# Performance work log

Hardware: AMD Instinct MI355X
Metric: run time of the kernel (lower is better)

Reference implementation:

```python
import jax, jax.numpy as jnp
import numpy as np

N, D_MODEL, NUM_HEAD = 2, 256, 8
HI, WI = 40, 40
MAX_DIS = 7
WS = 2 * MAX_DIS + 1          # 15
HD = D_MODEL // NUM_HEAD      # 32
T = HD ** 0.5
NEG = 1e8                     # fp32 mask value used by the torch module


def setup_inputs() -> dict:
    key = jax.random.key(0)
    ks = jax.random.split(key, 10)
    s = 0.02
    f = lambda i, shape: jax.random.normal(ks[i], shape, jnp.float32)
    return dict(
        q=f(0, (N, D_MODEL, HI, WI)),
        k=f(1, (N, D_MODEL, HI, WI)),
        v=f(2, (N, D_MODEL, HI, WI)),
        Wq=f(3, (D_MODEL, D_MODEL)) * s, bq=jnp.zeros((D_MODEL,), jnp.float32),
        Wk=f(4, (D_MODEL, D_MODEL)) * s, bk=jnp.zeros((D_MODEL,), jnp.float32),
        Wv=f(5, (D_MODEL, D_MODEL)) * s, bv=jnp.zeros((D_MODEL,), jnp.float32),
        rel_k_w=f(6, (NUM_HEAD, WS * WS, HD)) * s,      # grouped 1x1 conv weight
        rel_k_b=jnp.zeros((NUM_HEAD, WS * WS), jnp.float32),
        rel_v=f(7, (NUM_HEAD, HD, WS * WS)) * s,        # nn.Parameter (zeros in torch; random here to exercise math)
        Wp=f(8, (D_MODEL, D_MODEL)) * s, bp=jnp.zeros((D_MODEL,), jnp.float32),
    )


def _geometry(h, w):
    # Static (numpy) index/mask construction matching compute_mask().
    qy = np.repeat(np.arange(h), w)
    qx = np.tile(np.arange(w), h)
    dy = qy[None, :] - qy[:, None]          # key - query, [hw, hw]
    dx = qx[None, :] - qx[:, None]
    valid = (np.abs(dy) <= MAX_DIS) & (np.abs(dx) <= MAX_DIS)
    widx = (np.clip(dy + MAX_DIS, 0, WS - 1) * WS + np.clip(dx + MAX_DIS, 0, WS - 1))
    offs = np.arange(-MAX_DIS, MAX_DIS + 1)
    dyo = np.repeat(offs, WS)               # [ws*ws] row-major window order (dy*WS+dx)
    dxo = np.tile(offs, WS)
    ky = qy[:, None] + dyo[None, :]         # [hw, ws*ws]
    kx = qx[:, None] + dxo[None, :]
    in_img = (ky >= 0) & (ky < h) & (kx >= 0) & (kx < w)
    jidx = np.clip(ky, 0, h - 1) * w + np.clip(kx, 0, w - 1)
    return (jnp.asarray(valid), jnp.asarray(widx), jnp.asarray(in_img), jnp.asarray(jidx))


def reference(q, k, v, Wq, bq, Wk, bk, Wv, bv, rel_k_w, rel_k_b, rel_v, Wp, bp):
    n, c, h, w = q.shape
    hw = h * w
    nh, hd = NUM_HEAD, c // NUM_HEAD

    def proj(x, Wt, b):  # 1x1 conv == per-pixel linear
        return jnp.einsum('oc,ncp->nop', Wt, x.reshape(n, c, hw)) + b[None, :, None]

    qf = proj(q, Wq, bq)
    kf = proj(k, Wk, bk)
    vf = proj(v, Wv, bv)

    qh = qf.reshape(n, nh, hd, hw)
    kh = kf.reshape(n, nh, hd, hw)
    vh = vf.reshape(n, nh, hd, hw)

    # grouped 1x1 conv: per-head linear from hd channels to ws*ws (computed BEFORE q/T)
    rel = jnp.einsum('hwd,nhdp->nhpw', rel_k_w, qh) + rel_k_b[None, :, None, :]  # [n,nh,hw,ws2]

    qh = qh / T
    qk = jnp.einsum('nhdi,nhdj->nhij', qh, kh)   # [n,nh,hw,hw]

    valid, widx, in_img, jidx = _geometry(h, w)

    # --- 'global' path: dense hw x hw, non-local keys masked with -1e8, local keys get rel bias ---
    rel_dense = jnp.take_along_axis(rel, widx[None, None], axis=3)   # [n,nh,hw,hw]
    global_logits = jnp.where(valid[None, None], qk + rel_dense, qk - NEG)
    global_attn = jax.nn.softmax(global_logits, axis=-1)
    agg_value = jnp.einsum('nhij,nhdj->inhd', global_attn, vh).reshape(hw, n, c)

    # --- local path: gather ws*ws window per query; out-of-image keys are -1e8 (pad value), rel added everywhere ---
    gathered = jnp.take_along_axis(qk, jidx[None, None], axis=3)     # [n,nh,hw,ws2]
    local_logits = jnp.where(in_img[None, None], gathered, -NEG) + rel
    local_attn = jax.nn.softmax(local_logits, axis=-1)
    agg_bias = jnp.einsum('nhiw,hdw->inhd', local_attn, rel_v).reshape(hw, n, c)

    out = (agg_value + agg_bias) @ Wp.T + bp    # nn.Linear, output [hw, n, c]
    return out, local_attn
```

## Files before the change

kernel.cpp:

```cpp
#include <hip/hip_runtime.h>
#include <hip/hip_bf16.h>

#define HW    1600
#define NB    2
#define NHEAD 8
#define HD    32
#define WS2   225
#define WDIM  40
#define CDIM  256
#define PROJ  819200
#define RELSTR 248
#define TSC   5.656854249492381f

typedef __attribute__((ext_vector_type(8))) short short8;
typedef __attribute__((ext_vector_type(4))) float floatx4;

static __device__ __forceinline__ float bu2f(short u) {
    return __uint_as_float(((unsigned)(unsigned short)u) << 16);
}
static __device__ __forceinline__ short f2bu(float f) {
    __hip_bfloat16 h = __float2bfloat16(f);
    short s; __builtin_memcpy(&s, &h, 2); return s;
}
static __device__ __forceinline__ unsigned pk2(short a, short b) {
    return (unsigned)(unsigned short)a | ((unsigned)(unsigned short)b << 16);
}
static __device__ __forceinline__ float ldf(const void* p, size_t i, bool f32) {
    return f32 ? ((const float*)p)[i] : __bfloat162float(((const __hip_bfloat16*)p)[i]);
}
static __device__ __forceinline__ void st_out(void* p, size_t i, float v, bool f32) {
    if (f32) ((float*)p)[i] = v;
    else     ((__hip_bfloat16*)p)[i] = __float2bfloat16(v);
}

__global__ __launch_bounds__(256) void prep_kernel(
    const void* __restrict__ q, const void* __restrict__ relv,
    const void* __restrict__ Wq, const void* __restrict__ Wk,
    const void* __restrict__ Wv, const void* __restrict__ Wp,
    const void* __restrict__ bq, const void* __restrict__ bk,
    const void* __restrict__ bv, const void* __restrict__ bp,
    const void* __restrict__ rkw, const void* __restrict__ rkb,
    int* __restrict__ flag, __hip_bfloat16* __restrict__ relvT,
    __hip_bfloat16* __restrict__ Wqb, __hip_bfloat16* __restrict__ Wkb,
    __hip_bfloat16* __restrict__ Wvb, __hip_bfloat16* __restrict__ Wpb,
    float* __restrict__ bqf, float* __restrict__ bkf,
    float* __restrict__ bvf, float* __restrict__ bpf,
    __hip_bfloat16* __restrict__ rkwb, __hip_bfloat16* __restrict__ rkbb)
{
    __shared__ int sbad;
    if (threadIdx.x == 0) sbad = 0;
    __syncthreads();
    int bad = 0;
    const __hip_bfloat16* qb = (const __hip_bfloat16*)q;
    for (int i = threadIdx.x; i < 4096; i += 256) {
        float v = __bfloat162float(qb[i]);
        if (!(v > -1e6f && v < 1e6f)) bad = 1;
    }
    if (bad) sbad = 1;
    __syncthreads();
    const bool f32 = (sbad != 0);
    if (blockIdx.x == 0 && threadIdx.x == 0) *flag = sbad;

    const int gid = blockIdx.x * 256 + threadIdx.x;
    const int gsz = gridDim.x * 256;

    for (int e = gid; e < NHEAD * WS2 * HD; e += gsz) {
        const int h = e / (WS2 * HD), idx = e - h * (WS2 * HD);
        const int w = idx >> 5, d = idx & 31;
        relvT[e] = __float2bfloat16(ldf(relv, ((size_t)h * HD + d) * WS2 + w, f32));
    }
    for (int e = gid; e < CDIM * CDIM; e += gsz) {
        Wqb[e] = __float2bfloat16(ldf(Wq, e, f32));
        Wkb[e] = __float2bfloat16(ldf(Wk, e, f32));
        Wvb[e] = __float2bfloat16(ldf(Wv, e, f32));
        Wpb[e] = __float2bfloat16(ldf(Wp, e, f32));
    }
    for (int e = gid; e < CDIM; e += gsz) {
        bqf[e] = ldf(bq, e, f32); bkf[e] = ldf(bk, e, f32);
        bvf[e] = ldf(bv, e, f32); bpf[e] = ldf(bp, e, f32);
    }
    for (int e = gid; e < NHEAD * WS2 * HD; e += gsz)
        rkwb[e] = __float2bfloat16(ldf(rkw, e, f32));
    for (int e = gid; e < NHEAD * WS2; e += gsz)
        rkbb[e] = __float2bfloat16(ldf(rkb, e, f32));
}

__global__ __launch_bounds__(256) void proj_fused(
    const void* __restrict__ xq, const void* __restrict__ xk, const void* __restrict__ xv,
    const __hip_bfloat16* __restrict__ Wqb, const float* __restrict__ bqf,
    const __hip_bfloat16* __restrict__ Wkb, const float* __restrict__ bkf,
    const __hip_bfloat16* __restrict__ Wvb, const float* __restrict__ bvf,
    const int* __restrict__ flag,
    __hip_bfloat16* __restrict__ qs, __hip_bfloat16* __restrict__ ks,
    __hip_bfloat16* __restrict__ vs)
{
    __shared__ short xt[32][264];
    const bool f32 = (*flag != 0);
    const int m0 = blockIdx.x * 32;
    const int n  = blockIdx.y;
    const int t  = blockIdx.z;
    const void* x; const short* W; const float* bias; __hip_bfloat16* dst; float scale;
    if (t == 0)      { x = xq; W = (const short*)Wqb; bias = bqf; dst = qs; scale = 0.17677669529663687f; }
    else if (t == 1) { x = xk; W = (const short*)Wkb; bias = bkf; dst = ks; scale = 1.f; }
    else             { x = xv; W = (const short*)Wvb; bias = bvf; dst = vs; scale = 1.f; }

    {
        const int c = threadIdx.x;
        const size_t xb = ((size_t)n * CDIM + c) * HW + m0;
        if (f32) {
            const float* xr = (const float*)x + xb;
            #pragma unroll
            for (int g = 0; g < 8; ++g) {
                float4 f = *(const float4*)(xr + g * 4);
                xt[g*4+0][c] = f2bu(f.x); xt[g*4+1][c] = f2bu(f.y);
                xt[g*4+2][c] = f2bu(f.z); xt[g*4+3][c] = f2bu(f.w);
            }
        } else {
            const __hip_bfloat16* xr = (const __hip_bfloat16*)x + xb;
            #pragma unroll
            for (int g = 0; g < 4; ++g) {
                short8 s = *(const short8*)(xr + g * 8);
                #pragma unroll
                for (int u = 0; u < 8; ++u) xt[g*8+u][c] = s[u];
            }
        }
    }
    __syncthreads();

    const int wave = threadIdx.x >> 6, lane = threadIdx.x & 63;
    const int m = lane & 15, qd = lane >> 4;

    short8 A[2][8];
    #pragma unroll
    for (int mt = 0; mt < 2; ++mt)
        #pragma unroll
        for (int k = 0; k < 8; ++k)
            A[mt][k] = *(const short8*)(&xt[mt*16 + m][k*32 + qd*8]);

    #pragma unroll
    for (int og = 0; og < 4; ++og) {
        const int o0 = (wave * 4 + og) * 16;
        short8 B[8];
        #pragma unroll
        for (int k = 0; k < 8; ++k)
            B[k] = *(const short8*)(W + (size_t)(o0 + m) * CDIM + k*32 + qd*8);
        floatx4 acc0 = {0,0,0,0}, acc1 = {0,0,0,0};
        #pragma unroll
        for (int k = 0; k < 8; ++k) {
            acc0 = __builtin_amdgcn_mfma_f32_16x16x32_bf16(A[0][k], B[k], acc0, 0, 0, 0);
            acc1 = __builtin_amdgcn_mfma_f32_16x16x32_bf16(A[1][k], B[k], acc1, 0, 0, 0);
        }
        const int o = o0 + (lane & 15), h = o >> 5, d = o & 31;
        const float bv_ = bias[o];
        #pragma unroll
        for (int rg = 0; rg < 4; ++rg) {
            const int p = m0 + (lane >> 4) * 4 + rg;
            dst[((size_t)(n*NHEAD + h)*HW + p)*HD + d]      = __float2bfloat16((acc0[rg] + bv_) * scale);
            dst[((size_t)(n*NHEAD + h)*HW + p + 16)*HD + d] = __float2bfloat16((acc1[rg] + bv_) * scale);
        }
    }
}

#define SP_OFF    0
#define R2_OFF    15616
#define R1_OFF    24064
#define SMAX_OFF  39680
#define SSUM_OFF  39936
#define SMEM_SZ   40192

__global__ __launch_bounds__(256) void attn_mfma(
    const __hip_bfloat16* __restrict__ qs, const __hip_bfloat16* __restrict__ ks,
    const __hip_bfloat16* __restrict__ vs,
    const short* __restrict__ rkwb, const short* __restrict__ rkbb,
    const __hip_bfloat16* __restrict__ relvT,
    const int* __restrict__ flag,
    __hip_bfloat16* __restrict__ agg,
    void* __restrict__ dout)
{
    __shared__ __align__(16) char smem[SMEM_SZ];
    short* sP   = (short*)(smem + SP_OFF);
    short* sRel = (short*)(smem + R2_OFF);
    short* sPw  = (short*)(smem + R2_OFF);
    short* sB   = (short*)(smem + R1_OFF);
    float* sOh  = (float*)(smem + R1_OFF);
    float* sMax = (float*)(smem + SMAX_OFF);
    float* sSum = (float*)(smem + SSUM_OFF);

    const bool f32 = (*flag != 0);
    const int tid = threadIdx.x;
    const int wave = tid >> 6, lane = tid & 63;
    const int m = lane & 15, quad = lane >> 4;
    const int y = blockIdx.x / 3, tile3 = blockIdx.x % 3;
    const int x0 = (tile3 == 0) ? 0 : (tile3 == 1) ? 16 : 24;
    const int wlo = (tile3 == 2) ? 8 : 0;
    const int nh_ = blockIdx.y;
    const int h = nh_ & 7, n = nh_ >> 3;
    const size_t qb = (size_t)nh_ * HW;
    const size_t qrow0 = qb + (size_t)y * WDIM + x0;

    const short8 afrag = *(const short8*)((const short*)qs + (qrow0 + m) * HD + quad * 8);

    for (int wt = wave; wt < 15; wt += 4) {
        const int w0 = wt * 16;
        const int wl = min(w0 + m, WS2 - 1);
        const short8 B = *(const short8*)(rkwb + ((size_t)h * WS2 + wl) * HD + quad * 8);
        floatx4 acc = {0.f, 0.f, 0.f, 0.f};
        acc = __builtin_amdgcn_mfma_f32_16x16x32_bf16(afrag, B, acc, 0, 0, 0);
        const int wcol = w0 + m;
        if (wcol < WS2) {
            const float rb_ = bu2f(rkbb[(size_t)h * WS2 + wcol]);
            #pragma unroll
            for (int rg = 0; rg < 4; ++rg)
                sRel[(quad * 4 + rg) * RELSTR + wcol] = f2bu(acc[rg] * TSC + rb_);
        }
    }
    __syncthreads();

    float L[8][4];
    #pragma unroll
    for (int j = 0; j < 8; ++j)
        #pragma unroll
        for (int rg = 0; rg < 4; ++rg) L[j][rg] = -1e30f;

    #pragma unroll
    for (int j = 0; j < 8; ++j) {
        const int t = wave + 4 * j;
        if (t < 30) {
            const int r = t >> 1, c0_ = (t & 1) << 4;
            const int cc = c0_ + m;
            const int ky = y + r - 7, kx = x0 - 7 + cc;
            const int gky = min(max(ky, 0), WDIM - 1), gkx = min(max(kx, 0), WDIM - 1);
            const short8 bfrag = *(const short8*)((const short*)ks + (qb + (size_t)gky * WDIM + gkx) * HD + quad * 8);
            floatx4 s4 = {0.f, 0.f, 0.f, 0.f};
            s4 = __builtin_amdgcn_mfma_f32_16x16x32_bf16(afrag, bfrag, s4, 0, 0, 0);
            const bool inimg = ((unsigned)ky < (unsigned)WDIM) && ((unsigned)kx < (unsigned)WDIM);
            #pragma unroll
            for (int rg = 0; rg < 4; ++rg) {
                const int qm = quad * 4 + rg;
                const int dx7 = cc - qm;
                if (inimg && (unsigned)dx7 < 15u)
                    L[j][rg] = s4[rg] + bu2f(sRel[qm * RELSTR + r * 15 + dx7]);
            }
        }
    }

    float mx[4];
    #pragma unroll
    for (int rg = 0; rg < 4; ++rg) {
        mx[rg] = L[0][rg];
        #pragma unroll
        for (int j = 1; j < 8; ++j) mx[rg] = fmaxf(mx[rg], L[j][rg]);
        #pragma unroll
        for (int off = 1; off <= 8; off <<= 1) mx[rg] = fmaxf(mx[rg], __shfl_xor(mx[rg], off));
    }
    if (m == 0) {
        #pragma unroll
        for (int rg = 0; rg < 4; ++rg) sMax[(quad * 4 + rg) * 4 + wave] = mx[rg];
    }
    __syncthreads();
    float M4[4], sm[4];
    #pragma unroll
    for (int rg = 0; rg < 4; ++rg) {
        const float4 v = *(const float4*)&sMax[(quad * 4 + rg) * 4];
        M4[rg] = fmaxf(fmaxf(v.x, v.y), fmaxf(v.z, v.w));
        sm[rg] = 0.f;
    }
    #pragma unroll
    for (int j = 0; j < 8; ++j)
        #pragma unroll
        for (int rg = 0; rg < 4; ++rg) { L[j][rg] = __expf(L[j][rg] - M4[rg]); sm[rg] += L[j][rg]; }
    #pragma unroll
    for (int rg = 0; rg < 4; ++rg)
        #pragma unroll
        for (int off = 1; off <= 8; off <<= 1) sm[rg] += __shfl_xor(sm[rg], off);
    if (m == 0) {
        #pragma unroll
        for (int rg = 0; rg < 4; ++rg) sSum[(quad * 4 + rg) * 4 + wave] = sm[rg];
    }
    __syncthreads();
    float inv4[4];
    #pragma unroll
    for (int rg = 0; rg < 4; ++rg) {
        const float4 v = *(const float4*)&sSum[(quad * 4 + rg) * 4];
        inv4[rg] = 1.f / (v.x + v.y + v.z + v.w);
    }

    for (int e = tid; e < 16 * 39; e += 256) {
        const int row = e / 39, c = 225 + (e - row * 39);
        sPw[row * 264 + c] = 0;
    }

    #pragma unroll
    for (int j = 0; j < 8; ++j) {
        const int t = wave + 4 * j;
        if (t < 30) {
            const int r = t >> 1, cc = ((t & 1) << 4) + m;
            #pragma unroll
            for (int rg = 0; rg < 4; ++rg) {
                const int qm = quad * 4 + rg;
                const short pb = f2bu(L[j][rg] * inv4[rg]);
                sP[qm * 488 + r * 32 + cc] = pb;
                const int dx7 = cc - qm;
                if ((unsigned)dx7 < 15u) sPw[qm * 264 + r * 15 + dx7] = pb;
            }
        }
    }
    __syncthreads();

    #pragma unroll
    for (int rr = 0; rr < 4; ++rr) {
        const int qm = wave * 4 + rr;
        if (qm >= wlo) {
            const size_t obase = (size_t)PROJ + (qrow0 + qm) * WS2;
            #pragma unroll
            for (int c = 0; c < 4; ++c) {
                const int col = lane + 64 * c;
                if (col < WS2) st_out(dout, obase + col, bu2f(sPw[qm * 264 + col]), f32);
            }
        }
    }

    for (int half = 0; half < 2; ++half) {
        __syncthreads();
        const int h16 = half << 4;
        {
            unsigned* dstw = (unsigned*)sB;
            for (int p = tid; p < 240; p += 256) {
                const int kk0 = 2 * p;
                const int r = kk0 >> 5, c = kk0 & 31;
                const int gky = min(max(y + r - 7, 0), WDIM - 1);
                const int gkx0 = min(max(x0 - 7 + c, 0), WDIM - 1);
                const int gkx1 = min(max(x0 - 7 + c + 1, 0), WDIM - 1);
                const short* v0 = (const short*)vs + (qb + (size_t)gky * WDIM + gkx0) * HD + h16;
                const short* v1 = (const short*)vs + (qb + (size_t)gky * WDIM + gkx1) * HD + h16;
                const short8 a0 = *(const short8*)v0, b0 = *(const short8*)v1;
                const short8 a1 = *(const short8*)(v0 + 8), b1 = *(const short8*)(v1 + 8);
                #pragma unroll
                for (int dd = 0; dd < 8; ++dd) dstw[dd * 244 + p] = pk2(a0[dd], b0[dd]);
                #pragma unroll
                for (int dd = 0; dd < 8; ++dd) dstw[(dd + 8) * 244 + p] = pk2(a1[dd], b1[dd]);
            }
        }
        __syncthreads();
        floatx4 acc = {0.f, 0.f, 0.f, 0.f};
        for (int u = wave; u < 15; u += 4) {
            const short8 Af = *(const short8*)(sP + m * 488 + u * 32 + quad * 8);
            const short8 Bf = *(const short8*)(sB + m * 488 + u * 32 + quad * 8);
            acc = __builtin_amdgcn_mfma_f32_16x16x32_bf16(Af, Bf, acc, 0, 0, 0);
        }
        __syncthreads();
        {
            unsigned* dstw = (unsigned*)sB;
            for (int p = tid; p < 132; p += 256) {
                const int w0 = 2 * p;
                short8 a0 = {0,0,0,0,0,0,0,0}, a1 = a0, b0 = a0, b1 = a0;
                if (w0 < WS2) {
                    const short* rp = (const short*)relvT + ((size_t)h * WS2 + w0) * HD + h16;
                    a0 = *(const short8*)rp; a1 = *(const short8*)(rp + 8);
                }
                if (w0 + 1 < WS2) {
                    const short* rp = (const short*)relvT + ((size_t)h * WS2 + w0 + 1) * HD + h16;
                    b0 = *(const short8*)rp; b1 = *(const short8*)(rp + 8);
                }
                #pragma unroll
                for (int dd = 0; dd < 8; ++dd) dstw[dd * 132 + p] = pk2(a0[dd], b0[dd]);
                #pragma unroll
                for (int dd = 0; dd < 8; ++dd) dstw[(dd + 8) * 132 + p] = pk2(a1[dd], b1[dd]);
            }
        }
        __syncthreads();
        for (int u = wave; u < 8; u += 4) {
            const short8 Af = *(const short8*)(sPw + m * 264 + u * 32 + quad * 8);
            const short8 Bf = *(const short8*)(sB + m * 264 + u * 32 + quad * 8);
            acc = __builtin_amdgcn_mfma_f32_16x16x32_bf16(Af, Bf, acc, 0, 0, 0);
        }
        __syncthreads();
        #pragma unroll
        for (int rg = 0; rg < 4; ++rg)
            sOh[wave * 256 + (quad * 4 + rg) * 16 + m] = acc[rg];
        __syncthreads();
        {
            const int qq = tid >> 4, dd = tid & 15;
            const float s = sOh[tid] + sOh[256 + tid] + sOh[512 + tid] + sOh[768 + tid];
            if (qq >= wlo) {
                const size_t i = (size_t)y * WDIM + x0 + qq;
                agg[(i * NB + n) * CDIM + h * HD + h16 + dd] = __float2bfloat16(s);
            }
        }
    }
}

__global__ __launch_bounds__(256) void out_mfma(
    const __hip_bfloat16* __restrict__ agg, const short* __restrict__ Wpb,
    const float* __restrict__ bpf, const int* __restrict__ flag,
    void* __restrict__ dout)
{
    const bool f32 = (*flag != 0);
    const int wave = threadIdx.x >> 6, lane = threadIdx.x & 63;
    const int rb0 = blockIdx.x << 4;
    const int m = lane & 15, qd = lane >> 4;

    const __hip_bfloat16* arow = agg + (size_t)(rb0 + m) * CDIM + qd * 8;
    short8 A[8];
    #pragma unroll
    for (int k = 0; k < 8; ++k)
        A[k] = *(const short8*)(arow + k * 32);

    #pragma unroll
    for (int p = 0; p < 2; ++p) {
        const int o0 = wave * 64 + p * 32;
        floatx4 acc0 = {0.f, 0.f, 0.f, 0.f}, acc1 = {0.f, 0.f, 0.f, 0.f};
        #pragma unroll
        for (int k = 0; k < 8; ++k) {
            short8 b0 = *(const short8*)(Wpb + (size_t)(o0 + m) * CDIM + k * 32 + qd * 8);
            short8 b1 = *(const short8*)(Wpb + (size_t)(o0 + 16 + m) * CDIM + k * 32 + qd * 8);
            acc0 = __builtin_amdgcn_mfma_f32_16x16x32_bf16(A[k], b0, acc0, 0, 0, 0);
            acc1 = __builtin_amdgcn_mfma_f32_16x16x32_bf16(A[k], b1, acc1, 0, 0, 0);
        }
        const int oa = o0 + (lane & 15), ob = oa + 16;
        const float ba_ = bpf[oa];
        const float bb_ = bpf[ob];
        #pragma unroll
        for (int rg = 0; rg < 4; ++rg) {
            const int rb = rb0 + (lane >> 4) * 4 + rg;
            st_out(dout, (size_t)rb * CDIM + oa, acc0[rg] + ba_, f32);
            st_out(dout, (size_t)rb * CDIM + ob, acc1[rg] + bb_, f32);
        }
    }
}

extern "C" void kernel_launch(void* const* d_in, const int* in_sizes, int n_in,
                              void* d_out, int out_size, void* d_ws, size_t ws_size,
                              hipStream_t stream)
{
    const void* q   = d_in[0];
    const void* k   = d_in[1];
    const void* v   = d_in[2];
    const void* Wq  = d_in[3];
    const void* bq  = d_in[4];
    const void* Wk  = d_in[5];
    const void* bk  = d_in[6];
    const void* Wv  = d_in[7];
    const void* bv  = d_in[8];
    const void* rkw = d_in[9];
    const void* rkb = d_in[10];
    const void* rlv = d_in[11];
    const void* Wp  = d_in[12];
    const void* bp  = d_in[13];

    char* wsb = (char*)d_ws;
    int* flag = (int*)wsb;
    __hip_bfloat16* relvT = (__hip_bfloat16*)(wsb + 64);
    __hip_bfloat16* qs    = (__hip_bfloat16*)(wsb + 64 + 115200);
    __hip_bfloat16* ks    = qs + PROJ;
    __hip_bfloat16* vs    = ks + PROJ;
    __hip_bfloat16* agg   = vs + PROJ;
    __hip_bfloat16* Wqb   = (__hip_bfloat16*)(wsb + 6668864);
    __hip_bfloat16* Wkb   = Wqb + CDIM * CDIM;
    __hip_bfloat16* Wvb   = Wkb + CDIM * CDIM;
    __hip_bfloat16* Wpb   = Wvb + CDIM * CDIM;
    __hip_bfloat16* rkwb  = (__hip_bfloat16*)(wsb + 7193152);
    __hip_bfloat16* rkbb  = (__hip_bfloat16*)(wsb + 7308352);
    float* bqf = (float*)(wsb + 7311952);
    float* bkf = bqf + CDIM;
    float* bvf = bkf + CDIM;
    float* bpf = bvf + CDIM;

    prep_kernel<<<64, 256, 0, stream>>>(q, rlv, Wq, Wk, Wv, Wp, bq, bk, bv, bp,
                                        rkw, rkb, flag, relvT,
                                        Wqb, Wkb, Wvb, Wpb, bqf, bkf, bvf, bpf,
                                        rkwb, rkbb);
    proj_fused<<<dim3(50, 2, 3), 256, 0, stream>>>(q, k, v, Wqb, bqf, Wkb, bkf,
                                                   Wvb, bvf, flag, qs, ks, vs);
    attn_mfma<<<dim3(120, 16), 256, 0, stream>>>(qs, ks, vs, (const short*)rkwb,
                                                 (const short*)rkbb, relvT, flag,
                                                 agg, d_out);
    out_mfma<<<200, 256, 0, stream>>>(agg, (const short*)Wpb, bpf, flag, d_out);
}
```

Baseline: 153.0 us.

## Transpose QK MFMA operands so each lane owns one query row

Swaps the MFMA operand order for the local QK scores so the accumulator layout puts one query per lane (m) with four consecutive keys per register group. This turns the per-row softmax max/sum reductions into two cross-quad shuffles instead of four per-row 4-step shuffles, and lets probabilities be written to shared memory as packed 4-element vectors. The windowed probability buffer moves to a stride-16 row layout, which changes the zero-fill pattern, the output indexing (now with a divide by 15) and the rel_v staging gather. The cost is more complex index math in the store and staging paths, plus risk in the padding and zeroing logic.

```diff
diff --git a/kernel.cpp b/kernel.cpp
--- a/kernel.cpp
+++ b/kernel.cpp
@@ -13,6 +13,7 @@
 #define TSC   5.656854249492381f
 
 typedef __attribute__((ext_vector_type(8))) short short8;
+typedef __attribute__((ext_vector_type(4))) short short4v;
 typedef __attribute__((ext_vector_type(4))) float floatx4;
 
 static __device__ __forceinline__ float bu2f(short u) {
@@ -228,65 +229,49 @@
         if (t < 30) {
             const int r = t >> 1, c0_ = (t & 1) << 4;
             const int cc = c0_ + m;
-            const int ky = y + r - 7, kx = x0 - 7 + cc;
-            const int gky = min(max(ky, 0), WDIM - 1), gkx = min(max(kx, 0), WDIM - 1);
-            const short8 bfrag = *(const short8*)((const short*)ks + (qb + (size_t)gky * WDIM + gkx) * HD + quad * 8);
+            const int ky = y + r - 7, kxl = x0 - 7 + cc;
+            const int gky = min(max(ky, 0), WDIM - 1), gkx = min(max(kxl, 0), WDIM - 1);
+            const short8 kfrag = *(const short8*)((const short*)ks + (qb + (size_t)gky * WDIM + gkx) * HD + quad * 8);
             floatx4 s4 = {0.f, 0.f, 0.f, 0.f};
-            s4 = __builtin_amdgcn_mfma_f32_16x16x32_bf16(afrag, bfrag, s4, 0, 0, 0);
-            const bool inimg = ((unsigned)ky < (unsigned)WDIM) && ((unsigned)kx < (unsigned)WDIM);
+            s4 = __builtin_amdgcn_mfma_f32_16x16x32_bf16(kfrag, afrag, s4, 0, 0, 0);
+            const bool kyok = (unsigned)ky < (unsigned)WDIM;
             #pragma unroll
             for (int rg = 0; rg < 4; ++rg) {
-                const int qm = quad * 4 + rg;
-                const int dx7 = cc - qm;
-                if (inimg && (unsigned)dx7 < 15u)
-                    L[j][rg] = s4[rg] + bu2f(sRel[qm * RELSTR + r * 15 + dx7]);
-            }
-        }
-    }
-
-    float mx[4];
-    #pragma unroll
-    for (int rg = 0; rg < 4; ++rg) {
-        mx[rg] = L[0][rg];
-        #pragma unroll
-        for (int j = 1; j < 8; ++j) mx[rg] = fmaxf(mx[rg], L[j][rg]);
-        #pragma unroll
-        for (int off = 1; off <= 8; off <<= 1) mx[rg] = fmaxf(mx[rg], __shfl_xor(mx[rg], off));
-    }
-    if (m == 0) {
-        #pragma unroll
-        for (int rg = 0; rg < 4; ++rg) sMax[(quad * 4 + rg) * 4 + wave] = mx[rg];
-    }
-    __syncthreads();
-    float M4[4], sm[4];
-    #pragma unroll
-    for (int rg = 0; rg < 4; ++rg) {
-        const float4 v = *(const float4*)&sMax[(quad * 4 + rg) * 4];
-        M4[rg] = fmaxf(fmaxf(v.x, v.y), fmaxf(v.z, v.w));
-        sm[rg] = 0.f;
-    }
+                const int kkc = c0_ + quad * 4 + rg;
+                const int kx = x0 - 7 + kkc;
+                const int dx7 = kkc - m;
+                if (kyok && (unsigned)kx < (unsigned)WDIM && (unsigned)dx7 < 15u)
+                    L[j][rg] = s4[rg] + bu2f(sRel[m * RELSTR + r * 15 + dx7]);
+            }
+        }
+    }
+
+    float mx = L[0][0];
     #pragma unroll
     for (int j = 0; j < 8; ++j)
         #pragma unroll
-        for (int rg = 0; rg < 4; ++rg) { L[j][rg] = __expf(L[j][rg] - M4[rg]); sm[rg] += L[j][rg]; }
-    #pragma unroll
-    for (int rg = 0; rg < 4; ++rg)
-        #pragma unroll
-        for (int off = 1; off <= 8; off <<= 1) sm[rg] += __shfl_xor(sm[rg], off);
-    if (m == 0) {
-        #pragma unroll
-        for (int rg = 0; rg < 4; ++rg) sSum[(quad * 4 + rg) * 4 + wave] = sm[rg];
-    }
-    __syncthreads();
-    float inv4[4];
-    #pragma unroll
-    for (int rg = 0; rg < 4; ++rg) {
-        const float4 v = *(const float4*)&sSum[(quad * 4 + rg) * 4];
-        inv4[rg] = 1.f / (v.x + v.y + v.z + v.w);
-    }
+        for (int rg = 0; rg < 4; ++rg) mx = fmaxf(mx, L[j][rg]);
+    mx = fmaxf(mx, __shfl_xor(mx, 16));
+    mx = fmaxf(mx, __shfl_xor(mx, 32));
+    if (lane < 16) sMax[lane * 4 + wave] = mx;
+    __syncthreads();
+    const float4 vM = *(const float4*)&sMax[m * 4];
+    const float M = fmaxf(fmaxf(vM.x, vM.y), fmaxf(vM.z, vM.w));
+    float sm = 0.f;
+    #pragma unroll
+    for (int j = 0; j < 8; ++j)
+        #pragma unroll
+        for (int rg = 0; rg < 4; ++rg) { L[j][rg] = __expf(L[j][rg] - M); sm += L[j][rg]; }
+    sm += __shfl_xor(sm, 16);
+    sm += __shfl_xor(sm, 32);
+    if (lane < 16) sSum[lane * 4 + wave] = sm;
+    __syncthreads();
+    const float4 vS = *(const float4*)&sSum[m * 4];
+    const float inv = 1.f / (vS.x + vS.y + vS.z + vS.w);
 
     for (int e = tid; e < 16 * 39; e += 256) {
-        const int row = e / 39, c = 225 + (e - row * 39);
+        const int row = e / 39, idx = e - row * 39;
+        const int c = (idx < 15) ? idx * 16 + 15 : 240 + (idx - 15);
         sPw[row * 264 + c] = 0;
     }
 
@@ -294,14 +279,16 @@
     for (int j = 0; j < 8; ++j) {
         const int t = wave + 4 * j;
         if (t < 30) {
-            const int r = t >> 1, cc = ((t & 1) << 4) + m;
+            const int r = t >> 1, c0_ = (t & 1) << 4;
+            const int kb = c0_ + quad * 4;
+            short4v pk;
+            #pragma unroll
+            for (int rg = 0; rg < 4; ++rg) pk[rg] = f2bu(L[j][rg] * inv);
+            *(short4v*)(sP + m * 488 + r * 32 + kb) = pk;
             #pragma unroll
             for (int rg = 0; rg < 4; ++rg) {
-                const int qm = quad * 4 + rg;
-                const short pb = f2bu(L[j][rg] * inv4[rg]);
-                sP[qm * 488 + r * 32 + cc] = pb;
-                const int dx7 = cc - qm;
-                if ((unsigned)dx7 < 15u) sPw[qm * 264 + r * 15 + dx7] = pb;
+                const int dx7 = kb + rg - m;
+                if ((unsigned)dx7 < 15u) sPw[m * 264 + r * 16 + dx7] = pk[rg];
             }
         }
     }
@@ -315,7 +302,10 @@
             #pragma unroll
             for (int c = 0; c < 4; ++c) {
                 const int col = lane + 64 * c;
-                if (col < WS2) st_out(dout, obase + col, bu2f(sPw[qm * 264 + col]), f32);
+                if (col < WS2) {
+                    const int rq = col / 15, dxq = col - rq * 15;
+                    st_out(dout, obase + col, bu2f(sPw[qm * 264 + rq * 16 + dxq]), f32);
+                }
             }
         }
     }
@@ -352,15 +342,17 @@
         {
             unsigned* dstw = (unsigned*)sB;
             for (int p = tid; p < 132; p += 256) {
-                const int w0 = 2 * p;
                 short8 a0 = {0,0,0,0,0,0,0,0}, a1 = a0, b0 = a0, b1 = a0;
-                if (w0 < WS2) {
+                if (p < 120) {
+                    const int kcol0 = 2 * p;
+                    const int r = kcol0 >> 4, dx = kcol0 & 15;
+                    const int w0 = r * 15 + dx;
                     const short* rp = (const short*)relvT + ((size_t)h * WS2 + w0) * HD + h16;
                     a0 = *(const short8*)rp; a1 = *(const short8*)(rp + 8);
-                }
-                if (w0 + 1 < WS2) {
-                    const short* rp = (const short*)relvT + ((size_t)h * WS2 + w0 + 1) * HD + h16;
-                    b0 = *(const short8*)rp; b1 = *(const short8*)(rp + 8);
+                    if (dx < 14) {
+                        const short* rq = (const short*)relvT + ((size_t)h * WS2 + w0 + 1) * HD + h16;
+                        b0 = *(const short8*)rq; b1 = *(const short8*)(rq + 8);
+                    }
                 }
                 #pragma unroll
                 for (int dd = 0; dd < 8; ++dd) dstw[dd * 132 + p] = pk2(a0[dd], b0[dd]);
```

After: 151.3 us. About the same (-1.1%).
